# Optimization experiments

Measured on AMD Instinct MI355X. Metric: run time of the kernel, lower is better.

## Reference

```python
import jax, jax.numpy as jnp
import numpy as np

N_NODES = 100000
N_EDGES = 1600000
IN_DIM, HID_DIM, OUT_DIM = 256, 128, 128


def gcn_norm(edge_index, edge_weight, num_nodes):
    # Add self-loops with weight 1 (PyG GCNConv default fill_value=1.0)
    loop = jnp.arange(num_nodes, dtype=edge_index.dtype)
    src = jnp.concatenate([edge_index[0], loop])
    dst = jnp.concatenate([edge_index[1], loop])
    w = jnp.concatenate([edge_weight, jnp.ones((num_nodes,), edge_weight.dtype)])
    # Symmetric normalization: deg computed at destination over edge weights
    deg = jax.ops.segment_sum(w, dst, num_segments=num_nodes)
    dinv = jnp.where(deg > 0, jax.lax.rsqrt(deg), 0.0)
    norm = dinv[src] * w * dinv[dst]  # [E + N]
    return src, dst, norm


def gcn_conv(x, W, b, src, dst, norm, num_nodes):
    h = x @ W                                  # [N, out]
    msg = h[src] * norm[:, None]               # gather + scale, [E+N, out]
    out = jax.ops.segment_sum(msg, dst, num_segments=num_nodes)  # scatter-add
    return out + b


def setup_inputs() -> dict:
    key = jax.random.key(0)
    ks = jax.random.split(key, 8)
    x = jax.random.normal(ks[0], (N_NODES, IN_DIM), dtype=jnp.float32)
    edge_index = jax.random.randint(ks[1], (2, N_EDGES), 0, N_NODES, dtype=jnp.int64)
    edge_weight = jax.random.uniform(ks[2], (N_EDGES,), dtype=jnp.float32)
    s1 = 1.0 / np.sqrt(IN_DIM)
    s2 = 1.0 / np.sqrt(HID_DIM)
    W1 = jax.random.uniform(ks[3], (IN_DIM, HID_DIM), jnp.float32, -s1, s1)
    b1 = jnp.zeros((HID_DIM,), jnp.float32)
    W2 = jax.random.uniform(ks[4], (HID_DIM, OUT_DIM), jnp.float32, -s2, s2)
    b2 = jnp.zeros((OUT_DIM,), jnp.float32)
    return {"x": x, "edge_index": edge_index, "edge_weight": edge_weight,
            "W1": W1, "b1": b1, "W2": W2, "b2": b2}


def reference(x, edge_index, edge_weight, W1, b1, W2, b2):
    n = x.shape[0]
    src, dst, norm = gcn_norm(edge_index, edge_weight, n)
    h = jax.nn.relu(gcn_conv(x, W1, b1, src, dst, norm, n))
    out = gcn_conv(h, W2, b2, src, dst, norm, n)
    return out
```

## Files before the change

### kernel.cpp

```cpp
#include <hip/hip_runtime.h>
#include <stdint.h>

#define N_NODES 100000
#define N_EDGES 1600000
#define IN_DIM 256
#define HID_DIM 128
#define OUT_DIM 128

#define NBUCK 391
#define CHUNK 4096

typedef __attribute__((ext_vector_type(8))) short short8;
typedef __attribute__((ext_vector_type(4))) float floatx4;

__device__ __forceinline__ float bf2f(unsigned short u) {
    union { unsigned int i; float f; } v; v.i = ((unsigned int)u) << 16; return v.f;
}
__device__ __forceinline__ unsigned short f2bf(float f) {
    union { float fl; unsigned int i; } v; v.fl = f;
    unsigned int x = v.i;
    return (unsigned short)((x + 0x7fffu + ((x >> 16) & 1u)) >> 16);
}
__device__ __forceinline__ float bflo(unsigned int u) {
    union { unsigned int i; float f; } v; v.i = u << 16; return v.f;
}
__device__ __forceinline__ float bfhi(unsigned int u) {
    union { unsigned int i; float f; } v; v.i = u & 0xffff0000u; return v.f;
}
__device__ __forceinline__ float asf(unsigned int u) {
    union { unsigned int i; float f; } v; v.i = u; return v.f;
}
__device__ __forceinline__ unsigned int asu(float f) {
    union { float fl; unsigned int i; } v; v.fl = f; return v.i;
}
__device__ __forceinline__ unsigned int pack2(float a, float b) {
    unsigned int ua = asu(a), ub = asu(b);
    ua += 0x7fffu + ((ua >> 16) & 1u);
    ub += 0x7fffu + ((ub >> 16) & 1u);
    return (ua >> 16) | (ub & 0xffff0000u);
}
__device__ __forceinline__ short8 pack8(float4 a, float4 b) {
    union { unsigned int u[4]; short8 s; } r;
    r.u[0] = pack2(a.x, a.y);
    r.u[1] = pack2(a.z, a.w);
    r.u[2] = pack2(b.x, b.y);
    r.u[3] = pack2(b.z, b.w);
    return r.s;
}

__global__ void k_detect(const unsigned int* __restrict__ xu, const unsigned int* __restrict__ eu,
                         int* __restrict__ flags, int* __restrict__ bucket_cnt) {
    __shared__ int s_huge, s_odd;
    if (threadIdx.x == 0) { s_huge = 0; s_odd = 0; }
    if (threadIdx.x < NBUCK) bucket_cnt[threadIdx.x] = 0;
    __syncthreads();
    int huge = 0, odd = 0;
    for (int i = threadIdx.x; i < 1024; i += 512) {
        unsigned int b = xu[i];
        unsigned int e = (b >> 23) & 0xffu;
        if (e >= 0xf0u) huge = 1;
        if (eu[2 * i + 1] != 0) odd = 1;
    }
    if (huge) atomicOr(&s_huge, 1);
    if (odd) atomicOr(&s_odd, 1);
    __syncthreads();
    if (threadIdx.x == 0) { flags[0] = s_huge ? 0 : 1; flags[1] = s_odd ? 0 : 1; }
}

__device__ __forceinline__ int load_idx(const void* base, long long i, int i64m) {
    int v = i64m ? (int)((const long long*)base)[i] : ((const int*)base)[i];
    return v < 0 ? 0 : (v >= N_NODES ? N_NODES - 1 : v);
}
__device__ __forceinline__ float load_f(const void* base, long long i, int f32m) {
    return f32m ? ((const float*)base)[i] : bf2f(((const unsigned short*)base)[i]);
}

__global__ void k_bhist(const void* __restrict__ ei, const int* __restrict__ flags,
                        int* __restrict__ bucket_cnt, int e) {
    __shared__ int h[NBUCK];
    for (int t = threadIdx.x; t < NBUCK; t += 256) h[t] = 0;
    __syncthreads();
    int i64m = flags[1];
    int base = blockIdx.x * CHUNK;
    int end = base + CHUNK < e ? base + CHUNK : e;
    for (int i = base + threadIdx.x; i < end; i += 256) {
        int d = load_idx(ei, (long long)N_EDGES + i, i64m);
        atomicAdd(&h[d >> 8], 1);
    }
    __syncthreads();
    for (int t = threadIdx.x; t < NBUCK; t += 256)
        if (h[t]) atomicAdd(&bucket_cnt[t], h[t]);
}

__global__ void k_bscan(const int* __restrict__ bucket_cnt, int* __restrict__ bucket_base,
                        int* __restrict__ bucket_cursor, int* __restrict__ rowptr) {
    __shared__ int lds[512];
    int t = threadIdx.x;
    int v = (t < NBUCK) ? bucket_cnt[t] : 0;
    lds[t] = v;
    __syncthreads();
    for (int off = 1; off < 512; off <<= 1) {
        int x = (t >= off) ? lds[t - off] : 0;
        __syncthreads();
        lds[t] += x;
        __syncthreads();
    }
    int excl = lds[t] - v;
    if (t < NBUCK) { bucket_base[t] = excl; bucket_cursor[t] = excl; }
    if (t == 0) { bucket_base[NBUCK] = lds[NBUCK - 1]; rowptr[N_NODES] = N_EDGES; }
}

__global__ void k_bscatter(const void* __restrict__ ei, const void* __restrict__ ew,
                           const int* __restrict__ flags, int* __restrict__ bucket_cursor,
                           uint2* __restrict__ ebuf, int e) {
    __shared__ int h[NBUCK];
    for (int t = threadIdx.x; t < NBUCK; t += 256) h[t] = 0;
    __syncthreads();
    int f32m = flags[0], i64m = flags[1];
    int base = blockIdx.x * CHUNK;
    int end = base + CHUNK < e ? base + CHUNK : e;
    for (int i = base + threadIdx.x; i < end; i += 256) {
        int d = load_idx(ei, (long long)N_EDGES + i, i64m);
        atomicAdd(&h[d >> 8], 1);
    }
    __syncthreads();
    for (int t = threadIdx.x; t < NBUCK; t += 256) {
        int c = h[t];
        h[t] = c ? atomicAdd(&bucket_cursor[t], c) : 0;
    }
    __syncthreads();
    for (int i = base + threadIdx.x; i < end; i += 256) {
        int s = load_idx(ei, i, i64m);
        int d = load_idx(ei, (long long)N_EDGES + i, i64m);
        float w = load_f(ew, i, f32m);
        int b = d >> 8;
        int p = atomicAdd(&h[b], 1);
        uint2 c; c.x = (unsigned int)s | ((unsigned int)(d & 255) << 17); c.y = asu(w);
        ebuf[p] = c;
    }
}

__global__ void k_fine(const uint2* __restrict__ ebuf, const int* __restrict__ bucket_base,
                       uint2* __restrict__ csr, int* __restrict__ rowptr,
                       float* __restrict__ dinv, int n) {
    __shared__ int h[256];
    __shared__ float fw[256];
    __shared__ int c2[256];
    int t = threadIdx.x, b = blockIdx.x;
    int e0 = bucket_base[b], e1 = bucket_base[b + 1];
    h[t] = 0; fw[t] = 0.f;
    __syncthreads();
    for (int i = e0 + t; i < e1; i += 256) {
        uint2 c = ebuf[i];
        int dl = (c.x >> 17) & 255;
        atomicAdd(&h[dl], 1);
        atomicAdd(&fw[dl], asf(c.y));
    }
    __syncthreads();
    int own = h[t];
    for (int off = 1; off < 256; off <<= 1) {
        int x = (t >= off) ? h[t - off] : 0;
        __syncthreads();
        h[t] += x;
        __syncthreads();
    }
    int excl = h[t] - own;
    int node = (b << 8) + t;
    if (node < n) {
        rowptr[node] = e0 + excl;
        dinv[node] = rsqrtf(1.0f + fw[t]);
    }
    c2[t] = e0 + excl;
    __syncthreads();
    for (int i = e0 + t; i < e1; i += 256) {
        uint2 c = ebuf[i];
        int dl = (c.x >> 17) & 255;
        int p = atomicAdd(&c2[dl], 1);
        csr[p] = c;
    }
}

__global__ void k_fold(uint4* __restrict__ csr4, const float* __restrict__ dinv, int npair) {
    int i = blockIdx.x * 256 + threadIdx.x;
    if (i >= npair) return;
    uint4 c = csr4[i];
    c.y = asu(asf(c.y) * dinv[c.x & 0x1FFFF]);
    c.w = asu(asf(c.w) * dinv[c.z & 0x1FFFF]);
    csr4[i] = c;
}

__global__ void k_transpose(const void* __restrict__ W1, const void* __restrict__ W2,
                            const int* __restrict__ flags,
                            unsigned short* __restrict__ W1T, unsigned short* __restrict__ W2T) {
    int i = blockIdx.x * 256 + threadIdx.x;
    int f32m = flags[0];
    if (i < IN_DIM * HID_DIM) {
        int k = i / HID_DIM, n = i % HID_DIM;
        W1T[n * IN_DIM + k] = f2bf(load_f(W1, i, f32m));
    } else {
        int j = i - IN_DIM * HID_DIM;
        if (j < HID_DIM * OUT_DIM) {
            int k = j / OUT_DIM, n = j % OUT_DIM;
            W2T[n * HID_DIM + k] = f2bf(load_f(W2, j, f32m));
        }
    }
}

template <int KH, bool F32M>
__device__ __forceinline__ void gemm_loop(const void* __restrict__ A,
                                          const unsigned short* __restrict__ Bs,
                                          size_t aoff0, size_t aoff1,
                                          int quad, int l16, floatx4 (&acc)[2][8]) {
    constexpr int NCH = KH / 32;
    constexpr int BMASK = KH / 8 - 1;
    float4 fraw[2][2];
    short8 braw[2];
    if (F32M) {
        const float* ap = (const float*)A;
        fraw[0][0] = *(const float4*)(ap + aoff0);
        fraw[0][1] = *(const float4*)(ap + aoff0 + 4);
        fraw[1][0] = *(const float4*)(ap + aoff1);
        fraw[1][1] = *(const float4*)(ap + aoff1 + 4);
    } else {
        const unsigned short* ap = (const unsigned short*)A;
        braw[0] = *(const short8*)(ap + aoff0);
        braw[1] = *(const short8*)(ap + aoff1);
    }
#pragma unroll
    for (int ch = 0; ch < NCH; ch++) {
        float4 nf[2][2];
        short8 nb[2];
        if (ch + 1 < NCH) {
            int o = (ch + 1) * 32;
            if (F32M) {
                const float* ap = (const float*)A;
                nf[0][0] = *(const float4*)(ap + aoff0 + o);
                nf[0][1] = *(const float4*)(ap + aoff0 + o + 4);
                nf[1][0] = *(const float4*)(ap + aoff1 + o);
                nf[1][1] = *(const float4*)(ap + aoff1 + o + 4);
            } else {
                const unsigned short* ap = (const unsigned short*)A;
                nb[0] = *(const short8*)(ap + aoff0 + o);
                nb[1] = *(const short8*)(ap + aoff1 + o);
            }
        }
        short8 a0, a1;
        if (F32M) {
            a0 = pack8(fraw[0][0], fraw[0][1]);
            a1 = pack8(fraw[1][0], fraw[1][1]);
        } else {
            a0 = braw[0];
            a1 = braw[1];
        }
#pragma unroll
        for (int c = 0; c < 8; c++) {
            int col = c * 16 + l16;
            int boff = col * KH + 8 * ((ch * 4 + quad + (col & 7)) & BMASK);
            short8 bf = *(const short8*)(Bs + boff);
            acc[0][c] = __builtin_amdgcn_mfma_f32_16x16x32_bf16(a0, bf, acc[0][c], 0, 0, 0);
            acc[1][c] = __builtin_amdgcn_mfma_f32_16x16x32_bf16(a1, bf, acc[1][c], 0, 0, 0);
        }
        if (ch + 1 < NCH) {
            if (F32M) {
                fraw[0][0] = nf[0][0]; fraw[0][1] = nf[0][1];
                fraw[1][0] = nf[1][0]; fraw[1][1] = nf[1][1];
            } else {
                braw[0] = nb[0]; braw[1] = nb[1];
            }
        }
    }
}

template <int K, bool RAWA>
__global__ void k_gemm(const void* __restrict__ A, const unsigned short* __restrict__ WT,
                       unsigned short* __restrict__ H, const int* __restrict__ flags, int n) {
    constexpr int KH = (K > 128) ? 128 : K;
    __shared__ unsigned short Bs[128 * KH];

    int wave = threadIdx.x >> 6;
    int lane = threadIdx.x & 63;
    int quad = lane >> 4;
    int l16 = lane & 15;
    int rowbase = blockIdx.x * 128 + wave * 32;
    int r0 = rowbase + l16;        if (r0 >= n) r0 = n - 1;
    int r1 = rowbase + 16 + l16;   if (r1 >= n) r1 = n - 1;
    size_t aoff0 = (size_t)r0 * K + quad * 8;
    size_t aoff1 = (size_t)r1 * K + quad * 8;

    floatx4 acc[2][8];
#pragma unroll
    for (int t = 0; t < 2; t++)
#pragma unroll
        for (int c = 0; c < 8; c++) acc[t][c] = (floatx4){0.f, 0.f, 0.f, 0.f};

    int f32m = RAWA ? flags[0] : 0;

#pragma unroll
    for (int hh = 0; hh < K / KH; hh++) {
        if (hh) __syncthreads();
        for (int base = threadIdx.x * 8; base < 128 * KH; base += 256 * 8) {
            int col = base / KH;
            int k = base - col * KH;
            int ks = (k + (col & 7) * 8) & (KH - 1);
            *(short8*)(&Bs[col * KH + ks]) = *(const short8*)(WT + col * K + hh * KH + k);
        }
        __syncthreads();
        if (RAWA && f32m)
            gemm_loop<KH, true>(A, Bs, aoff0 + hh * KH, aoff1 + hh * KH, quad, l16, acc);
        else
            gemm_loop<KH, false>(A, Bs, aoff0 + hh * KH, aoff1 + hh * KH, quad, l16, acc);
    }

#pragma unroll
    for (int t = 0; t < 2; t++)
#pragma unroll
        for (int c = 0; c < 8; c++)
#pragma unroll
            for (int r = 0; r < 4; r++) {
                int grow = rowbase + t * 16 + quad * 4 + r;
                if (grow < n) H[(size_t)grow * 128 + c * 16 + l16] = f2bf(acc[t][c][r]);
            }
}

__device__ __forceinline__ void acc8(float wt, uint4 hv, float* a) {
    a[0] += wt * bflo(hv.x); a[1] += wt * bfhi(hv.x);
    a[2] += wt * bflo(hv.y); a[3] += wt * bfhi(hv.y);
    a[4] += wt * bflo(hv.z); a[5] += wt * bfhi(hv.z);
    a[6] += wt * bflo(hv.w); a[7] += wt * bfhi(hv.w);
}

template <bool RELU, bool FINAL>
__global__ void k_aggregate(const unsigned short* __restrict__ H, const int* __restrict__ rowptr,
                            const uint2* __restrict__ csr, const float* __restrict__ dinv,
                            const void* __restrict__ bias, void* __restrict__ out,
                            const int* __restrict__ flags, int n) {
    int node = blockIdx.x * 16 + (threadIdx.x >> 4);
    int lane = threadIdx.x & 15;
    if (node >= n) return;
    int col = lane * 8;
    int f32m = flags[0];

    int e0 = rowptr[node], e1 = rowptr[node + 1];
    uint4 u = *(const uint4*)(H + (size_t)node * 128 + col);
    float dn = dinv[node];

    float a[8] = {0.f, 0.f, 0.f, 0.f, 0.f, 0.f, 0.f, 0.f};

    const uint2* ep = csr + e0;
    int nb = (e1 - e0) >> 2;
    uint2 c0, c1, c2, c3;
    uint4 h0, h1, h2, h3;
    if (nb) {
        c0 = ep[0]; c1 = ep[1]; c2 = ep[2]; c3 = ep[3];
        h0 = *(const uint4*)(H + (size_t)(c0.x & 0x1FFFF) * 128 + col);
        h1 = *(const uint4*)(H + (size_t)(c1.x & 0x1FFFF) * 128 + col);
        h2 = *(const uint4*)(H + (size_t)(c2.x & 0x1FFFF) * 128 + col);
        h3 = *(const uint4*)(H + (size_t)(c3.x & 0x1FFFF) * 128 + col);
    }
    for (int b = 1; b < nb; b++) {
        const uint2* np = ep + 4 * b;
        uint2 d0 = np[0], d1 = np[1], d2 = np[2], d3 = np[3];
        uint4 g0 = *(const uint4*)(H + (size_t)(d0.x & 0x1FFFF) * 128 + col);
        uint4 g1 = *(const uint4*)(H + (size_t)(d1.x & 0x1FFFF) * 128 + col);
        uint4 g2 = *(const uint4*)(H + (size_t)(d2.x & 0x1FFFF) * 128 + col);
        uint4 g3 = *(const uint4*)(H + (size_t)(d3.x & 0x1FFFF) * 128 + col);
        acc8(asf(c0.y), h0, a); acc8(asf(c1.y), h1, a);
        acc8(asf(c2.y), h2, a); acc8(asf(c3.y), h3, a);
        c0 = d0; c1 = d1; c2 = d2; c3 = d3;
        h0 = g0; h1 = g1; h2 = g2; h3 = g3;
    }
    if (nb) {
        acc8(asf(c0.y), h0, a); acc8(asf(c1.y), h1, a);
        acc8(asf(c2.y), h2, a); acc8(asf(c3.y), h3, a);
    }
    for (int e = e0 + (nb << 2); e < e1; e++) {
        uint2 c = csr[e];
        uint4 hh = *(const uint4*)(H + (size_t)(c.x & 0x1FFFF) * 128 + col);
        acc8(asf(c.y), hh, a);
    }

    float coef = dn * dn;
    a[0] = dn * a[0] + coef * bflo(u.x) + load_f(bias, col, f32m);
    a[1] = dn * a[1] + coef * bfhi(u.x) + load_f(bias, col + 1, f32m);
    a[2] = dn * a[2] + coef * bflo(u.y) + load_f(bias, col + 2, f32m);
    a[3] = dn * a[3] + coef * bfhi(u.y) + load_f(bias, col + 3, f32m);
    a[4] = dn * a[4] + coef * bflo(u.z) + load_f(bias, col + 4, f32m);
    a[5] = dn * a[5] + coef * bfhi(u.z) + load_f(bias, col + 5, f32m);
    a[6] = dn * a[6] + coef * bflo(u.w) + load_f(bias, col + 6, f32m);
    a[7] = dn * a[7] + coef * bfhi(u.w) + load_f(bias, col + 7, f32m);

    if (RELU) {
#pragma unroll
        for (int i = 0; i < 8; i++) a[i] = fmaxf(a[i], 0.f);
    }
    if (FINAL && f32m) {
        float* op = (float*)out + (size_t)node * 128 + col;
        float4 o0 = {a[0], a[1], a[2], a[3]};
        float4 o1 = {a[4], a[5], a[6], a[7]};
        *(float4*)op = o0;
        *(float4*)(op + 4) = o1;
    } else {
        uint4 o;
        o.x = pack2(a[0], a[1]); o.y = pack2(a[2], a[3]);
        o.z = pack2(a[4], a[5]); o.w = pack2(a[6], a[7]);
        *(uint4*)((unsigned short*)out + (size_t)node * 128 + col) = o;
    }
}

extern "C" void kernel_launch(void* const* d_in, const int* in_sizes, int n_in,
                              void* d_out, int out_size, void* d_ws, size_t ws_size,
                              hipStream_t stream) {
    const void* x  = d_in[0];
    const void* ei = d_in[1];
    const void* ew = d_in[2];
    const void* W1 = d_in[3];
    const void* b1 = d_in[4];
    const void* W2 = d_in[5];
    const void* b2 = d_in[6];

    char* p = (char*)d_ws;
    auto alloc = [&](size_t bytes) { char* r = p; p += (bytes + 255) & ~(size_t)255; return r; };
    int*   flags    = (int*)alloc(256);
    float* dinv     = (float*)alloc((size_t)N_NODES * 4);
    int*   rowptr   = (int*)alloc((size_t)(N_NODES + 1) * 4);
    int*   bucket_cnt    = (int*)alloc((size_t)NBUCK * 4);
    int*   bucket_base   = (int*)alloc((size_t)(NBUCK + 1) * 4);
    int*   bucket_cursor = (int*)alloc((size_t)NBUCK * 4);
    uint2* csr      = (uint2*)alloc((size_t)N_EDGES * 8);
    unsigned short* W1T  = (unsigned short*)alloc((size_t)IN_DIM * HID_DIM * 2);
    unsigned short* W2T  = (unsigned short*)alloc((size_t)HID_DIM * OUT_DIM * 2);
    unsigned short* hbuf = (unsigned short*)alloc((size_t)N_NODES * 128 * 2);
    unsigned short* zbuf = (unsigned short*)alloc((size_t)N_NODES * 128 * 2);
    uint2* ebuf = (uint2*)hbuf;

    int nbC = (N_EDGES + CHUNK - 1) / CHUNK;
    int nbG = (N_NODES + 127) / 128;
    int nbA = (N_NODES + 15) / 16;
    int nbF = (N_EDGES / 2 + 255) / 256;

    k_detect<<<1, 512, 0, stream>>>((const unsigned int*)x, (const unsigned int*)ei, flags, bucket_cnt);
    k_bhist<<<nbC, 256, 0, stream>>>(ei, flags, bucket_cnt, N_EDGES);
    k_bscan<<<1, 512, 0, stream>>>(bucket_cnt, bucket_base, bucket_cursor, rowptr);
    k_bscatter<<<nbC, 256, 0, stream>>>(ei, ew, flags, bucket_cursor, ebuf, N_EDGES);
    k_fine<<<NBUCK, 256, 0, stream>>>(ebuf, bucket_base, csr, rowptr, dinv, N_NODES);
    k_fold<<<nbF, 256, 0, stream>>>((uint4*)csr, dinv, N_EDGES / 2);
    k_transpose<<<(IN_DIM * HID_DIM + HID_DIM * OUT_DIM + 255) / 256, 256, 0, stream>>>(W1, W2, flags, W1T, W2T);

    k_gemm<IN_DIM, true><<<nbG, 256, 0, stream>>>(x, W1T, hbuf, flags, N_NODES);
    k_aggregate<true, false><<<nbA, 256, 0, stream>>>(hbuf, rowptr, csr, dinv,
                                                      b1, zbuf, flags, N_NODES);
    k_gemm<HID_DIM, false><<<nbG, 256, 0, stream>>>(zbuf, W2T, hbuf, flags, N_NODES);
    k_aggregate<false, true><<<nbA, 256, 0, stream>>>(hbuf, rowptr, csr, dinv,
                                                      b2, d_out, flags, N_NODES);
}
```

Baseline: 465.7 us.

## Use block-local dynamic node scheduling in aggregation kernel

Each aggregation block now owns 64 nodes, and 16-lane groups claim nodes one at a time through a shared-memory atomic cursor. This balances the uneven per-node degree work within a block instead of giving each group exactly one node. Bias values are loaded once per thread and reused across nodes. The gather loop drops the software-pipelined prefetch for a simpler 4-wide loop, which may expose more load latency, and the per-node atomic plus shuffle add overhead.

```diff
diff --git a/kernel.cpp b/kernel.cpp
--- a/kernel.cpp
+++ b/kernel.cpp
@@ -322,6 +322,8 @@
             }
 }
 
+#define NODES_PER_BLK 64
+
 __device__ __forceinline__ void acc8(float wt, uint4 hv, float* a) {
     a[0] += wt * bflo(hv.x); a[1] += wt * bfhi(hv.x);
     a[2] += wt * bflo(hv.y); a[3] += wt * bfhi(hv.y);
@@ -334,76 +336,72 @@
                             const uint2* __restrict__ csr, const float* __restrict__ dinv,
                             const void* __restrict__ bias, void* __restrict__ out,
                             const int* __restrict__ flags, int n) {
-    int node = blockIdx.x * 16 + (threadIdx.x >> 4);
+    __shared__ int cursor;
+    if (threadIdx.x == 0) cursor = 0;
+    __syncthreads();
     int lane = threadIdx.x & 15;
-    if (node >= n) return;
     int col = lane * 8;
     int f32m = flags[0];
 
-    int e0 = rowptr[node], e1 = rowptr[node + 1];
-    uint4 u = *(const uint4*)(H + (size_t)node * 128 + col);
-    float dn = dinv[node];
-
-    float a[8] = {0.f, 0.f, 0.f, 0.f, 0.f, 0.f, 0.f, 0.f};
-
-    const uint2* ep = csr + e0;
-    int nb = (e1 - e0) >> 2;
-    uint2 c0, c1, c2, c3;
-    uint4 h0, h1, h2, h3;
-    if (nb) {
-        c0 = ep[0]; c1 = ep[1]; c2 = ep[2]; c3 = ep[3];
-        h0 = *(const uint4*)(H + (size_t)(c0.x & 0x1FFFF) * 128 + col);
-        h1 = *(const uint4*)(H + (size_t)(c1.x & 0x1FFFF) * 128 + col);
-        h2 = *(const uint4*)(H + (size_t)(c2.x & 0x1FFFF) * 128 + col);
-        h3 = *(const uint4*)(H + (size_t)(c3.x & 0x1FFFF) * 128 + col);
-    }
-    for (int b = 1; b < nb; b++) {
-        const uint2* np = ep + 4 * b;
-        uint2 d0 = np[0], d1 = np[1], d2 = np[2], d3 = np[3];
-        uint4 g0 = *(const uint4*)(H + (size_t)(d0.x & 0x1FFFF) * 128 + col);
-        uint4 g1 = *(const uint4*)(H + (size_t)(d1.x & 0x1FFFF) * 128 + col);
-        uint4 g2 = *(const uint4*)(H + (size_t)(d2.x & 0x1FFFF) * 128 + col);
-        uint4 g3 = *(const uint4*)(H + (size_t)(d3.x & 0x1FFFF) * 128 + col);
-        acc8(asf(c0.y), h0, a); acc8(asf(c1.y), h1, a);
-        acc8(asf(c2.y), h2, a); acc8(asf(c3.y), h3, a);
-        c0 = d0; c1 = d1; c2 = d2; c3 = d3;
-        h0 = g0; h1 = g1; h2 = g2; h3 = g3;
-    }
-    if (nb) {
-        acc8(asf(c0.y), h0, a); acc8(asf(c1.y), h1, a);
-        acc8(asf(c2.y), h2, a); acc8(asf(c3.y), h3, a);
-    }
-    for (int e = e0 + (nb << 2); e < e1; e++) {
-        uint2 c = csr[e];
-        uint4 hh = *(const uint4*)(H + (size_t)(c.x & 0x1FFFF) * 128 + col);
-        acc8(asf(c.y), hh, a);
-    }
-
-    float coef = dn * dn;
-    a[0] = dn * a[0] + coef * bflo(u.x) + load_f(bias, col, f32m);
-    a[1] = dn * a[1] + coef * bfhi(u.x) + load_f(bias, col + 1, f32m);
-    a[2] = dn * a[2] + coef * bflo(u.y) + load_f(bias, col + 2, f32m);
-    a[3] = dn * a[3] + coef * bfhi(u.y) + load_f(bias, col + 3, f32m);
-    a[4] = dn * a[4] + coef * bflo(u.z) + load_f(bias, col + 4, f32m);
-    a[5] = dn * a[5] + coef * bfhi(u.z) + load_f(bias, col + 5, f32m);
-    a[6] = dn * a[6] + coef * bflo(u.w) + load_f(bias, col + 6, f32m);
-    a[7] = dn * a[7] + coef * bfhi(u.w) + load_f(bias, col + 7, f32m);
-
-    if (RELU) {
-#pragma unroll
-        for (int i = 0; i < 8; i++) a[i] = fmaxf(a[i], 0.f);
-    }
-    if (FINAL && f32m) {
-        float* op = (float*)out + (size_t)node * 128 + col;
-        float4 o0 = {a[0], a[1], a[2], a[3]};
-        float4 o1 = {a[4], a[5], a[6], a[7]};
-        *(float4*)op = o0;
-        *(float4*)(op + 4) = o1;
-    } else {
-        uint4 o;
-        o.x = pack2(a[0], a[1]); o.y = pack2(a[2], a[3]);
-        o.z = pack2(a[4], a[5]); o.w = pack2(a[6], a[7]);
-        *(uint4*)((unsigned short*)out + (size_t)node * 128 + col) = o;
+    float bv[8];
+#pragma unroll
+    for (int i = 0; i < 8; i++) bv[i] = load_f(bias, col + i, f32m);
+
+    for (;;) {
+        int idx;
+        if (lane == 0) idx = atomicAdd(&cursor, 1);
+        idx = __shfl(idx, 0, 16);
+        if (idx >= NODES_PER_BLK) break;
+        int node = blockIdx.x * NODES_PER_BLK + idx;
+        if (node >= n) break;
+
+        int e0 = rowptr[node], e1 = rowptr[node + 1];
+        uint4 u = *(const uint4*)(H + (size_t)node * 128 + col);
+        float dn = dinv[node];
+
+        float a[8] = {0.f, 0.f, 0.f, 0.f, 0.f, 0.f, 0.f, 0.f};
+        int e = e0;
+        for (; e + 4 <= e1; e += 4) {
+            uint2 c0 = csr[e], c1 = csr[e + 1], c2 = csr[e + 2], c3 = csr[e + 3];
+            uint4 h0 = *(const uint4*)(H + (size_t)(c0.x & 0x1FFFF) * 128 + col);
+            uint4 h1 = *(const uint4*)(H + (size_t)(c1.x & 0x1FFFF) * 128 + col);
+            uint4 h2 = *(const uint4*)(H + (size_t)(c2.x & 0x1FFFF) * 128 + col);
+            uint4 h3 = *(const uint4*)(H + (size_t)(c3.x & 0x1FFFF) * 128 + col);
+            acc8(asf(c0.y), h0, a); acc8(asf(c1.y), h1, a);
+            acc8(asf(c2.y), h2, a); acc8(asf(c3.y), h3, a);
+        }
+        for (; e < e1; e++) {
+            uint2 c = csr[e];
+            uint4 hh = *(const uint4*)(H + (size_t)(c.x & 0x1FFFF) * 128 + col);
+            acc8(asf(c.y), hh, a);
+        }
+
+        float coef = dn * dn;
+        a[0] = dn * a[0] + coef * bflo(u.x) + bv[0];
+        a[1] = dn * a[1] + coef * bfhi(u.x) + bv[1];
+        a[2] = dn * a[2] + coef * bflo(u.y) + bv[2];
+        a[3] = dn * a[3] + coef * bfhi(u.y) + bv[3];
+        a[4] = dn * a[4] + coef * bflo(u.z) + bv[4];
+        a[5] = dn * a[5] + coef * bfhi(u.z) + bv[5];
+        a[6] = dn * a[6] + coef * bflo(u.w) + bv[6];
+        a[7] = dn * a[7] + coef * bfhi(u.w) + bv[7];
+
+        if (RELU) {
+#pragma unroll
+            for (int i = 0; i < 8; i++) a[i] = fmaxf(a[i], 0.f);
+        }
+        if (FINAL && f32m) {
+            float* op = (float*)out + (size_t)node * 128 + col;
+            float4 o0 = {a[0], a[1], a[2], a[3]};
+            float4 o1 = {a[4], a[5], a[6], a[7]};
+            *(float4*)op = o0;
+            *(float4*)(op + 4) = o1;
+        } else {
+            uint4 o;
+            o.x = pack2(a[0], a[1]); o.y = pack2(a[2], a[3]);
+            o.z = pack2(a[4], a[5]); o.w = pack2(a[6], a[7]);
+            *(uint4*)((unsigned short*)out + (size_t)node * 128 + col) = o;
+        }
     }
 }
 
@@ -435,7 +433,7 @@
 
     int nbC = (N_EDGES + CHUNK - 1) / CHUNK;
     int nbG = (N_NODES + 127) / 128;
-    int nbA = (N_NODES + 15) / 16;
+    int nbA = (N_NODES + NODES_PER_BLK - 1) / NODES_PER_BLK;
     int nbF = (N_EDGES / 2 + 255) / 256;
 
     k_detect<<<1, 512, 0, stream>>>((const unsigned int*)x, (const unsigned int*)ei, flags, bucket_cnt);
```

New measurement: 454.4 us. -2.4%, faster.
